# Kernel optimization log

Measured on AMD Instinct MI355X. Metric: run time of the kernel, lower is better.

The kernel has to match this reference:

```python
import jax, jax.numpy as jnp
import numpy as np

N = 2048
EMBED_DIM = 64
N_SUBJ, N_REL, N_OBJ = 16, 9, 16


def setup_inputs() -> dict:
    key = jax.random.key(0)
    ks = jax.random.split(key, 16)
    scale = 0.05  # keep sigmoid unsaturated
    return {
        "subj_idx": jax.random.randint(ks[0], (N,), 0, N_SUBJ, dtype=jnp.int32),
        "rel_idx": jax.random.randint(ks[1], (N,), 0, N_REL, dtype=jnp.int32),
        "obj_idx": jax.random.randint(ks[2], (N,), 0, N_OBJ, dtype=jnp.int32),
        "subj_table": jax.random.normal(ks[3], (N_SUBJ, EMBED_DIM), jnp.float32),
        "rel_table": jax.random.normal(ks[4], (N_REL, EMBED_DIM), jnp.float32),
        "obj_table": jax.random.normal(ks[5], (N_OBJ, EMBED_DIM), jnp.float32),
        "proj_w": jax.random.normal(ks[6], (EMBED_DIM, 3 * EMBED_DIM), jnp.float32) * scale,
        "proj_b": jax.random.normal(ks[7], (EMBED_DIM,), jnp.float32) * scale,
        "w1": jax.random.normal(ks[8], (EMBED_DIM, 2 * EMBED_DIM), jnp.float32) * scale,
        "b1": jax.random.normal(ks[9], (EMBED_DIM,), jnp.float32) * scale,
        "w2": jax.random.normal(ks[10], (32, EMBED_DIM), jnp.float32) * scale,
        "b2": jax.random.normal(ks[11], (32,), jnp.float32) * scale,
        "w3": jax.random.normal(ks[12], (1, 32), jnp.float32) * scale,
        "b3": jax.random.normal(ks[13], (1,), jnp.float32) * scale,
    }


def reference(subj_idx, rel_idx, obj_idx, subj_table, rel_table, obj_table,
              proj_w, proj_b, w1, b1, w2, b2, w3, b3):
    # --- ClaimEmbedder.embed, batched over all N claims ---
    # combined [N, 3*D] = cat(subj, rel, obj) embeddings; proj -> [N, D]
    combined = jnp.concatenate(
        [subj_table[subj_idx], rel_table[rel_idx], obj_table[obj_idx]], axis=-1)
    e = combined @ proj_w.T + proj_b  # [N, D]

    # --- conflict_scorer over all ordered pairs (i, j) ---
    # Linear(2D -> D) on cat(e_i, e_j) == e_i @ W1a.T + e_j @ W1b.T + b1
    d = e.shape[-1]
    w1a, w1b = w1[:, :d], w1[:, d:]
    hi = e @ w1a.T          # [N, D] contribution of left claim
    hj = e @ w1b.T          # [N, D] contribution of right claim
    h = jax.nn.relu(hi[:, None, :] + hj[None, :, :] + b1)  # [N, N, D]
    # Dropout(0.1) is identity in eval / no_grad inference.
    h2 = jax.nn.relu(jnp.einsum('ijd,kd->ijk', h, w2) + b2)  # [N, N, 32]
    scores = jax.nn.sigmoid(jnp.einsum('ijk,k->ij', h2, w3[0]) + b3[0])  # [N, N]
    # Only pairs with i < j are scored in the original nested loop.
    return jnp.triu(scores, k=1)
```

## Files before the change

kernel.cpp:

```cpp
#include <hip/hip_runtime.h>
#include <hip/hip_bf16.h>

#define NROWS 2048
#define HH 72

typedef __attribute__((ext_vector_type(4))) float f32x4;
typedef _Float16 f16x2 __attribute__((ext_vector_type(2)));
typedef _Float16 f16x8 __attribute__((ext_vector_type(8)));
typedef __fp16 fp16x2_raw __attribute__((ext_vector_type(2)));

union H8 { f16x8 v; f16x2 h2[4]; };

static __device__ __forceinline__ f32x4 vmax0(f32x4 a) {
    return __builtin_elementwise_max(a, (f32x4)0.f);
}
static __device__ __forceinline__ f16x8 hmax0(f16x8 a) {
    return __builtin_elementwise_max(a, (f16x8)(_Float16)0.f);
}
static __device__ __forceinline__ f16x2 pkrtz(float a, float b) {
    union { fp16x2_raw r; f16x2 f; } c;
    c.r = __builtin_amdgcn_cvt_pkrtz(a, b);
    return c.f;
}

#define TJ_OFF  2688

__global__ __launch_bounds__(256) void tab_kernel(
    const float* __restrict__ subj_table, const float* __restrict__ rel_table,
    const float* __restrict__ obj_table,
    const float* __restrict__ proj_w, const float* __restrict__ proj_b,
    const float* __restrict__ w1, const float* __restrict__ b1,
    float* __restrict__ ws)
{
    __shared__ float et[64];
    const int b = blockIdx.x;
    const int side = b & 1;
    const int r = b >> 1;
    const int tid = threadIdx.x;
    const int lane = tid & 63;
    const int w = tid >> 6;

    if (r == 41) {
        if (tid < 64) et[tid] = proj_b[tid];
    } else {
        const float* src; int off;
        if (r < 16)      { src = subj_table + r * 64;        off = 0;   }
        else if (r < 25) { src = rel_table + (r - 16) * 64;  off = 64;  }
        else             { src = obj_table + (r - 25) * 64;  off = 128; }
        const float sv = src[lane];
        #pragma unroll
        for (int t = 0; t < 4; ++t) {
            const int d0 = w * 16 + t * 4;
            float p0 = sv * proj_w[(d0 + 0) * 192 + off + lane];
            float p1 = sv * proj_w[(d0 + 1) * 192 + off + lane];
            float p2 = sv * proj_w[(d0 + 2) * 192 + off + lane];
            float p3 = sv * proj_w[(d0 + 3) * 192 + off + lane];
            #pragma unroll
            for (int m = 1; m < 64; m <<= 1) {
                p0 += __shfl_xor(p0, m, 64);
                p1 += __shfl_xor(p1, m, 64);
                p2 += __shfl_xor(p2, m, 64);
                p3 += __shfl_xor(p3, m, 64);
            }
            if (lane == 0) {
                et[d0 + 0] = p0; et[d0 + 1] = p1;
                et[d0 + 2] = p2; et[d0 + 3] = p3;
            }
        }
    }
    __syncthreads();

    float* dst = ws + (side ? TJ_OFF : 0);
    const float sv2 = et[lane];
    const int woff = side * 64;
    #pragma unroll
    for (int t = 0; t < 4; ++t) {
        const int d0 = w * 16 + t * 4;
        float p0 = sv2 * w1[(d0 + 0) * 128 + woff + lane];
        float p1 = sv2 * w1[(d0 + 1) * 128 + woff + lane];
        float p2 = sv2 * w1[(d0 + 2) * 128 + woff + lane];
        float p3 = sv2 * w1[(d0 + 3) * 128 + woff + lane];
        #pragma unroll
        for (int m = 1; m < 64; m <<= 1) {
            p0 += __shfl_xor(p0, m, 64);
            p1 += __shfl_xor(p1, m, 64);
            p2 += __shfl_xor(p2, m, 64);
            p3 += __shfl_xor(p3, m, 64);
        }
        if (lane == 0) {
            const bool cst = (side == 0) && (r == 41);
            dst[r * 64 + d0 + 0] = p0 + (cst ? b1[d0 + 0] : 0.f);
            dst[r * 64 + d0 + 1] = p1 + (cst ? b1[d0 + 1] : 0.f);
            dst[r * 64 + d0 + 2] = p2 + (cst ? b1[d0 + 2] : 0.f);
            dst[r * 64 + d0 + 3] = p3 + (cst ? b1[d0 + 3] : 0.f);
        }
    }
}

#define PSTR 68

__global__ __launch_bounds__(256, 4) void pair_kernel(
    const int* __restrict__ subj_idx, const int* __restrict__ rel_idx,
    const int* __restrict__ obj_idx,
    const float* __restrict__ tab,
    const float* __restrict__ w2, const float* __restrict__ b2,
    const float* __restrict__ w3, const float* __restrict__ b3,
    float* __restrict__ out)
{
    const int bx = blockIdx.x, by = blockIdx.y;
    const int i0 = by * 32, j0 = bx * 32;
    const int tid = threadIdx.x;

    if (bx < by) {
        const float4 z = {0.f, 0.f, 0.f, 0.f};
        ((float4*)(out + (size_t)(i0 + (tid >> 3)) * NROWS + j0))[tid & 7] = z;
        return;
    }

    __shared__ _Float16 hiL[32 * HH];
    __shared__ _Float16 hjL[32 * HH];
    __shared__ float part[4 * 16 * PSTR];

    const int lane = tid & 63;
    const int wid  = tid >> 6;
    const int col  = lane & 15;
    const int quad = lane >> 4;
    const int wj   = wid & 1;
    const int wi   = wid >> 1;

    {
        const int rr = tid >> 3;
        const int cc = (tid & 7) * 8;
        const int iR = i0 + rr, jR = j0 + rr;
        const int si = subj_idx[iR], ri = 16 + rel_idx[iR], oi = 25 + obj_idx[iR];
        const int sj = subj_idx[jR], rj = 16 + rel_idx[jR], oj = 25 + obj_idx[jR];
        const float* TI = tab;
        const float* TJ = tab + TJ_OFF;
        const f32x4 v0 = *(const f32x4*)(TI + si * 64 + cc)
                       + *(const f32x4*)(TI + ri * 64 + cc)
                       + *(const f32x4*)(TI + oi * 64 + cc)
                       + *(const f32x4*)(TI + 41 * 64 + cc);
        const f32x4 v1 = *(const f32x4*)(TI + si * 64 + cc + 4)
                       + *(const f32x4*)(TI + ri * 64 + cc + 4)
                       + *(const f32x4*)(TI + oi * 64 + cc + 4)
                       + *(const f32x4*)(TI + 41 * 64 + cc + 4);
        H8 hp;
        hp.h2[0] = pkrtz(v0[0], v0[1]); hp.h2[1] = pkrtz(v0[2], v0[3]);
        hp.h2[2] = pkrtz(v1[0], v1[1]); hp.h2[3] = pkrtz(v1[2], v1[3]);
        *(f16x8*)&hiL[rr * HH + cc] = hp.v;

        const f32x4 u0 = *(const f32x4*)(TJ + sj * 64 + cc)
                       + *(const f32x4*)(TJ + rj * 64 + cc)
                       + *(const f32x4*)(TJ + oj * 64 + cc)
                       + *(const f32x4*)(TJ + 41 * 64 + cc);
        const f32x4 u1 = *(const f32x4*)(TJ + sj * 64 + cc + 4)
                       + *(const f32x4*)(TJ + rj * 64 + cc + 4)
                       + *(const f32x4*)(TJ + oj * 64 + cc + 4)
                       + *(const f32x4*)(TJ + 41 * 64 + cc + 4);
        H8 hq;
        hq.h2[0] = pkrtz(u0[0], u0[1]); hq.h2[1] = pkrtz(u0[2], u0[3]);
        hq.h2[2] = pkrtz(u1[0], u1[1]); hq.h2[3] = pkrtz(u1[2], u1[3]);
        *(f16x8*)&hjL[rr * HH + cc] = hq.v;
    }

    H8 wf[2][2];
    #pragma unroll
    for (int ch = 0; ch < 2; ++ch)
        #pragma unroll
        for (int ks = 0; ks < 2; ++ks) {
            const f32x4* wr = (const f32x4*)(w2 + (ch * 16 + col) * 64 + ks * 32 + quad * 8);
            const f32x4 w0 = wr[0], w1v = wr[1];
            wf[ch][ks].h2[0] = pkrtz(w0[0], w0[1]);
            wf[ch][ks].h2[1] = pkrtz(w0[2], w0[3]);
            wf[ch][ks].h2[2] = pkrtz(w1v[0], w1v[1]);
            wf[ch][ks].h2[3] = pkrtz(w1v[2], w1v[3]);
        }
    const f32x4 b2A = *(const f32x4*)(b2 + quad * 4);
    const f32x4 b2B = *(const f32x4*)(b2 + 16 + quad * 4);
    const f32x4 w3A = *(const f32x4*)(w3 + quad * 4);
    const f32x4 w3B = *(const f32x4*)(w3 + 16 + quad * 4);
    const float b3v = b3[0];

    __syncthreads();

    const int hjb = (wj * 16 + col) * HH + quad * 8;
    const f16x8 hj0 = *(const f16x8*)&hjL[hjb];
    const f16x8 hj1 = *(const f16x8*)&hjL[hjb + 32];

    float* mypart = &part[wid * 16 * PSTR];

    #pragma unroll 8
    for (int it = 0; it < 16; ++it) {
        const int base = (wi * 16 + it) * HH + quad * 8;
        const f16x8 x0 = *(const f16x8*)&hiL[base];
        const f16x8 x1 = *(const f16x8*)&hiL[base + 32];

        const f16x8 f0 = hmax0(x0 + hj0);
        const f16x8 f1 = hmax0(x1 + hj1);

        f32x4 accA = b2A;
        f32x4 accB = b2B;
        accA = __builtin_amdgcn_mfma_f32_16x16x32_f16(wf[0][0].v, f0, accA, 0, 0, 0);
        accA = __builtin_amdgcn_mfma_f32_16x16x32_f16(wf[0][1].v, f1, accA, 0, 0, 0);
        accB = __builtin_amdgcn_mfma_f32_16x16x32_f16(wf[1][0].v, f0, accB, 0, 0, 0);
        accB = __builtin_amdgcn_mfma_f32_16x16x32_f16(wf[1][1].v, f1, accB, 0, 0, 0);

        const f32x4 ra = vmax0(accA);
        const f32x4 rb = vmax0(accB);
        const f32x4 t4 = ra * w3A + rb * w3B;
        mypart[it * PSTR + quad * 16 + col] = (t4[0] + t4[1]) + (t4[2] + t4[3]);
    }

    {
        const int sub = lane & 3;
        const int itx = lane >> 2;
        const float* pr = &mypart[itx * PSTR + sub * 4];
        const f32x4 s = *(const f32x4*)(pr)
                      + *(const f32x4*)(pr + 16)
                      + *(const f32x4*)(pr + 32)
                      + *(const f32x4*)(pr + 48);
        const int i  = i0 + wi * 16 + itx;
        const int jb = j0 + wj * 16 + sub * 4;
        float4 o;
        o.x = (jb + 0 > i) ? 1.f / (1.f + __expf(-(s[0] + b3v))) : 0.f;
        o.y = (jb + 1 > i) ? 1.f / (1.f + __expf(-(s[1] + b3v))) : 0.f;
        o.z = (jb + 2 > i) ? 1.f / (1.f + __expf(-(s[2] + b3v))) : 0.f;
        o.w = (jb + 3 > i) ? 1.f / (1.f + __expf(-(s[3] + b3v))) : 0.f;
        *(float4*)(out + (size_t)i * NROWS + jb) = o;
    }
}

extern "C" void kernel_launch(void* const* d_in, const int* in_sizes, int n_in,
                              void* d_out, int out_size, void* d_ws, size_t ws_size,
                              hipStream_t stream) {
    const int*   subj_idx   = (const int*)d_in[0];
    const int*   rel_idx    = (const int*)d_in[1];
    const int*   obj_idx    = (const int*)d_in[2];
    const float* subj_table = (const float*)d_in[3];
    const float* rel_table  = (const float*)d_in[4];
    const float* obj_table  = (const float*)d_in[5];
    const float* proj_w     = (const float*)d_in[6];
    const float* proj_b     = (const float*)d_in[7];
    const float* w1         = (const float*)d_in[8];
    const float* b1         = (const float*)d_in[9];
    const float* w2         = (const float*)d_in[10];
    const float* b2         = (const float*)d_in[11];
    const float* w3         = (const float*)d_in[12];
    const float* b3         = (const float*)d_in[13];
    float* out = (float*)d_out;
    float* ws  = (float*)d_ws;

    tab_kernel<<<dim3(84), dim3(256), 0, stream>>>(
        subj_table, rel_table, obj_table, proj_w, proj_b, w1, b1, ws);

    pair_kernel<<<dim3(NROWS / 32, NROWS / 32), dim3(256), 0, stream>>>(
        subj_idx, rel_idx, obj_idx, ws, w2, b2, w3, b3, out);
}
```

Measured before the change: 115.9 us.

## Precompute fp16 hi/hj rows in a separate gather kernel, read directly from global

Adds a kernel that gathers the per-claim hi and hj vectors once, sums the table rows, converts them to fp16 and stores them in the workspace. The pair kernel then loads its fp16 rows straight from global memory instead of gathering, summing and staging them through LDS, which also removes the __syncthreads. This is meant to cut redundant gather work repeated across every tile and the LDS staging and barrier. In exchange it adds a kernel launch, and each block's inner loop now reads global memory (likely served from L2 or cache) rather than LDS.

```diff
diff --git a/kernel.cpp b/kernel.cpp
--- a/kernel.cpp
+++ b/kernel.cpp
@@ -2,7 +2,6 @@
 #include <hip/hip_bf16.h>
 
 #define NROWS 2048
-#define HH 72
 
 typedef __attribute__((ext_vector_type(4))) float f32x4;
 typedef _Float16 f16x2 __attribute__((ext_vector_type(2)));
@@ -23,7 +22,8 @@
     return c.f;
 }
 
-#define TJ_OFF  2688
+#define TJ_OFF   2688
+#define H16_OFF  5376
 
 __global__ __launch_bounds__(256) void tab_kernel(
     const float* __restrict__ subj_table, const float* __restrict__ rel_table,
@@ -97,12 +97,54 @@
     }
 }
 
+__global__ __launch_bounds__(256) void hgather_kernel(
+    const int* __restrict__ subj_idx, const int* __restrict__ rel_idx,
+    const int* __restrict__ obj_idx, float* __restrict__ ws)
+{
+    _Float16* hi16 = (_Float16*)(ws + H16_OFF);
+    _Float16* hj16 = hi16 + NROWS * 64;
+    const float* TI = ws;
+    const float* TJ = ws + TJ_OFF;
+
+    const int t = threadIdx.x;
+    const int n = blockIdx.x * 32 + (t >> 3);
+    const int c = (t & 7) * 8;
+
+    const int s = subj_idx[n];
+    const int r = 16 + rel_idx[n];
+    const int o = 25 + obj_idx[n];
+
+    const f32x4 v0 = *(const f32x4*)(TI + s * 64 + c)
+                   + *(const f32x4*)(TI + r * 64 + c)
+                   + *(const f32x4*)(TI + o * 64 + c)
+                   + *(const f32x4*)(TI + 41 * 64 + c);
+    const f32x4 v1 = *(const f32x4*)(TI + s * 64 + c + 4)
+                   + *(const f32x4*)(TI + r * 64 + c + 4)
+                   + *(const f32x4*)(TI + o * 64 + c + 4)
+                   + *(const f32x4*)(TI + 41 * 64 + c + 4);
+    H8 hp;
+    hp.h2[0] = pkrtz(v0[0], v0[1]); hp.h2[1] = pkrtz(v0[2], v0[3]);
+    hp.h2[2] = pkrtz(v1[0], v1[1]); hp.h2[3] = pkrtz(v1[2], v1[3]);
+    *(f16x8*)&hi16[(size_t)n * 64 + c] = hp.v;
+
+    const f32x4 u0 = *(const f32x4*)(TJ + s * 64 + c)
+                   + *(const f32x4*)(TJ + r * 64 + c)
+                   + *(const f32x4*)(TJ + o * 64 + c)
+                   + *(const f32x4*)(TJ + 41 * 64 + c);
+    const f32x4 u1 = *(const f32x4*)(TJ + s * 64 + c + 4)
+                   + *(const f32x4*)(TJ + r * 64 + c + 4)
+                   + *(const f32x4*)(TJ + o * 64 + c + 4)
+                   + *(const f32x4*)(TJ + 41 * 64 + c + 4);
+    H8 hq;
+    hq.h2[0] = pkrtz(u0[0], u0[1]); hq.h2[1] = pkrtz(u0[2], u0[3]);
+    hq.h2[2] = pkrtz(u1[0], u1[1]); hq.h2[3] = pkrtz(u1[2], u1[3]);
+    *(f16x8*)&hj16[(size_t)n * 64 + c] = hq.v;
+}
+
 #define PSTR 68
 
 __global__ __launch_bounds__(256, 4) void pair_kernel(
-    const int* __restrict__ subj_idx, const int* __restrict__ rel_idx,
-    const int* __restrict__ obj_idx,
-    const float* __restrict__ tab,
+    const float* __restrict__ ws,
     const float* __restrict__ w2, const float* __restrict__ b2,
     const float* __restrict__ w3, const float* __restrict__ b3,
     float* __restrict__ out)
@@ -117,9 +159,10 @@
         return;
     }
 
-    __shared__ _Float16 hiL[32 * HH];
-    __shared__ _Float16 hjL[32 * HH];
     __shared__ float part[4 * 16 * PSTR];
+
+    const _Float16* hi16 = (const _Float16*)(ws + H16_OFF);
+    const _Float16* hj16 = hi16 + NROWS * 64;
 
     const int lane = tid & 63;
     const int wid  = tid >> 6;
@@ -128,40 +171,9 @@
     const int wj   = wid & 1;
     const int wi   = wid >> 1;
 
-    {
-        const int rr = tid >> 3;
-        const int cc = (tid & 7) * 8;
-        const int iR = i0 + rr, jR = j0 + rr;
-        const int si = subj_idx[iR], ri = 16 + rel_idx[iR], oi = 25 + obj_idx[iR];
-        const int sj = subj_idx[jR], rj = 16 + rel_idx[jR], oj = 25 + obj_idx[jR];
-        const float* TI = tab;
-        const float* TJ = tab + TJ_OFF;
-        const f32x4 v0 = *(const f32x4*)(TI + si * 64 + cc)
-                       + *(const f32x4*)(TI + ri * 64 + cc)
-                       + *(const f32x4*)(TI + oi * 64 + cc)
-                       + *(const f32x4*)(TI + 41 * 64 + cc);
-        const f32x4 v1 = *(const f32x4*)(TI + si * 64 + cc + 4)
-                       + *(const f32x4*)(TI + ri * 64 + cc + 4)
-                       + *(const f32x4*)(TI + oi * 64 + cc + 4)
-                       + *(const f32x4*)(TI + 41 * 64 + cc + 4);
-        H8 hp;
-        hp.h2[0] = pkrtz(v0[0], v0[1]); hp.h2[1] = pkrtz(v0[2], v0[3]);
-        hp.h2[2] = pkrtz(v1[0], v1[1]); hp.h2[3] = pkrtz(v1[2], v1[3]);
-        *(f16x8*)&hiL[rr * HH + cc] = hp.v;
-
-        const f32x4 u0 = *(const f32x4*)(TJ + sj * 64 + cc)
-                       + *(const f32x4*)(TJ + rj * 64 + cc)
-                       + *(const f32x4*)(TJ + oj * 64 + cc)
-                       + *(const f32x4*)(TJ + 41 * 64 + cc);
-        const f32x4 u1 = *(const f32x4*)(TJ + sj * 64 + cc + 4)
-                       + *(const f32x4*)(TJ + rj * 64 + cc + 4)
-                       + *(const f32x4*)(TJ + oj * 64 + cc + 4)
-                       + *(const f32x4*)(TJ + 41 * 64 + cc + 4);
-        H8 hq;
-        hq.h2[0] = pkrtz(u0[0], u0[1]); hq.h2[1] = pkrtz(u0[2], u0[3]);
-        hq.h2[2] = pkrtz(u1[0], u1[1]); hq.h2[3] = pkrtz(u1[2], u1[3]);
-        *(f16x8*)&hjL[rr * HH + cc] = hq.v;
-    }
+    const _Float16* hjr = hj16 + (size_t)(j0 + wj * 16 + col) * 64 + quad * 8;
+    const f16x8 hj0 = *(const f16x8*)(hjr);
+    const f16x8 hj1 = *(const f16x8*)(hjr + 32);
 
     H8 wf[2][2];
     #pragma unroll
@@ -181,29 +193,21 @@
     const f32x4 w3B = *(const f32x4*)(w3 + 16 + quad * 4);
     const float b3v = b3[0];
 
-    __syncthreads();
-
-    const int hjb = (wj * 16 + col) * HH + quad * 8;
-    const f16x8 hj0 = *(const f16x8*)&hjL[hjb];
-    const f16x8 hj1 = *(const f16x8*)&hjL[hjb + 32];
-
     float* mypart = &part[wid * 16 * PSTR];
+    const _Float16* hibase = hi16 + (size_t)(i0 + wi * 16) * 64 + quad * 8;
 
     #pragma unroll 8
     for (int it = 0; it < 16; ++it) {
-        const int base = (wi * 16 + it) * HH + quad * 8;
-        const f16x8 x0 = *(const f16x8*)&hiL[base];
-        const f16x8 x1 = *(const f16x8*)&hiL[base + 32];
+        const f16x8 x0 = *(const f16x8*)(hibase + it * 64);
+        const f16x8 x1 = *(const f16x8*)(hibase + it * 64 + 32);
 
         const f16x8 f0 = hmax0(x0 + hj0);
         const f16x8 f1 = hmax0(x1 + hj1);
 
-        f32x4 accA = b2A;
-        f32x4 accB = b2B;
-        accA = __builtin_amdgcn_mfma_f32_16x16x32_f16(wf[0][0].v, f0, accA, 0, 0, 0);
-        accA = __builtin_amdgcn_mfma_f32_16x16x32_f16(wf[0][1].v, f1, accA, 0, 0, 0);
-        accB = __builtin_amdgcn_mfma_f32_16x16x32_f16(wf[1][0].v, f0, accB, 0, 0, 0);
-        accB = __builtin_amdgcn_mfma_f32_16x16x32_f16(wf[1][1].v, f1, accB, 0, 0, 0);
+        f32x4 accA = __builtin_amdgcn_mfma_f32_16x16x32_f16(wf[0][0].v, f0, b2A, 0, 0, 0);
+        accA       = __builtin_amdgcn_mfma_f32_16x16x32_f16(wf[0][1].v, f1, accA, 0, 0, 0);
+        f32x4 accB = __builtin_amdgcn_mfma_f32_16x16x32_f16(wf[1][0].v, f0, b2B, 0, 0, 0);
+        accB       = __builtin_amdgcn_mfma_f32_16x16x32_f16(wf[1][1].v, f1, accB, 0, 0, 0);
 
         const f32x4 ra = vmax0(accA);
         const f32x4 rb = vmax0(accB);
@@ -253,6 +257,9 @@
     tab_kernel<<<dim3(84), dim3(256), 0, stream>>>(
         subj_table, rel_table, obj_table, proj_w, proj_b, w1, b1, ws);
 
+    hgather_kernel<<<dim3(NROWS / 32), dim3(256), 0, stream>>>(
+        subj_idx, rel_idx, obj_idx, ws);
+
     pair_kernel<<<dim3(NROWS / 32, NROWS / 32), dim3(256), 0, stream>>>(
-        subj_idx, rel_idx, obj_idx, ws, w2, b2, w3, b3, out);
-}
+        ws, w2, b2, w3, b3, out);
+}
```

After: 128.6 us. 1.11x slower.
